# Optimization experiments

Hardware: AMD Instinct MI355X
Metric: run time of the kernel (lower is better)

The kernel has to match this reference:

```python
import jax, jax.numpy as jnp
import numpy as np

EPS = 1e-5
COORD_TAU, COORD_KAPPA = 1.0, 1.0
COT_TAU, COT_LAM = 0.8, 0.7
GATE_FLOOR = 0.05


def _gconv(x, w, b=None):
    # grouped 1x1 conv: x [B,C,H,W], w [g, co_per_g, ci_per_g]
    B, C, H, W = x.shape
    g, co, ci = w.shape
    y = jnp.einsum('goi,bgihw->bgohw', w, x.reshape(B, g, ci, H, W)).reshape(B, g * co, H, W)
    return y if b is None else y + b[None, :, None, None]


def _conv1x1(x, w):
    # dense 1x1 conv: w [Cout, Cin]
    return jnp.einsum('oi,bihw->bohw', w, x)


def _inorm(x, g, b):
    # InstanceNorm2d(affine=True): per (B,C) stats over spatial dims, biased var
    mu = x.mean(axis=(2, 3), keepdims=True)
    var = x.var(axis=(2, 3), keepdims=True)
    return (x - mu) * jax.lax.rsqrt(var + EPS) * g[None, :, None, None] + b[None, :, None, None]


def _axis_softmax(z, L, axis):
    # stabilized softmax along a spatial axis, mean-rescaled by L
    zz = z / COORD_TAU
    zz = zz - zz.max(axis=axis, keepdims=True)
    return jax.nn.softmax(zz, axis=axis) * L


def _forward(x, compress_w, inc_g, inc_b, coord_proj_w, coord_proj_g, coord_proj_b,
             coord_h_w, coord_h_b, coord_wc_w, coord_wc_b, coord_alpha, coord_beta,
             cot_key_w, cot_val_w, cot_att1_w, cot_attn_g, cot_attn_b, cot_att2_w,
             cot_fuse_w, fusion_w, fus_g, fus_b, gate_w, expand_w):
    xc = jax.nn.relu(_inorm(_conv1x1(x, compress_w), inc_g, inc_b))  # [B,m,H,W]
    B, C, H, W = xc.shape

    # ---- Coord2H branch (use_softmax=True path) ----
    def proj(t):
        return jax.nn.silu(_inorm(_gconv(t, coord_proj_w), coord_proj_g, coord_proj_b))

    zh = _gconv(proj(xc.mean(axis=3, keepdims=True)), coord_h_w, coord_h_b)   # [B,C,H,1]
    zw = _gconv(proj(xc.mean(axis=2, keepdims=True)), coord_wc_w, coord_wc_b)  # [B,C,1,W]
    ah = _axis_softmax(zh, H, 2)
    aw = _axis_softmax(zw, W, 3)
    w_lin = coord_alpha * ah + coord_beta * aw  # broadcasts to [B,C,H,W]
    coord_out = xc * (1.0 + COORD_KAPPA * (w_lin - 1.0))

    # ---- CoT branch ----
    k1 = _gconv(xc, cot_key_w)
    v = _gconv(xc, cot_val_w)
    y = jnp.concatenate([k1, xc], axis=1)  # [B,2C,H,W]
    att = jax.nn.relu(_inorm(_gconv(y, cot_att1_w), cot_attn_g, cot_attn_b))
    att_logits = _gconv(att, cot_att2_w)
    z = (att_logits / COT_TAU).reshape(B, C, H * W)
    sm = jax.nn.softmax(z - z.max(axis=-1, keepdims=True), axis=-1).reshape(B, C, H, W) * (H * W)
    att_mix = (1.0 - COT_LAM) * jax.nn.sigmoid(att_logits) + COT_LAM * sm
    cot_out = _conv1x1(k1 + att_mix * v, cot_fuse_w)

    # ---- fusion + gate + expand ----
    fused = jax.nn.relu(_inorm(_conv1x1(jnp.concatenate([coord_out, cot_out], axis=1), fusion_w), fus_g, fus_b))
    gate = jax.nn.sigmoid(jnp.einsum('oi,bi->bo', gate_w, fused.mean(axis=(2, 3))))[:, :, None, None]  # [B,1,1,1]
    return _conv1x1(fused * (gate * (1.0 - GATE_FLOOR) + GATE_FLOOR), expand_w)


def setup_inputs() -> dict:
    key = jax.random.key(0)
    B, DIM, H, W = 8, 512, 128, 128
    RED, G = 16, 4
    m = DIM // RED  # 32
    mg = m // G     # 8
    ks = jax.random.split(key, 23)

    def n(k, s, sc=0.05):
        return jax.random.normal(k, s, dtype=jnp.float32) * sc

    return {
        'x': jax.random.normal(ks[0], (B, DIM, H, W), dtype=jnp.float32),
        'compress_w': n(ks[1], (m, DIM)),
        'inc_g': 1.0 + n(ks[2], (m,)),
        'inc_b': n(ks[3], (m,)),
        'coord_proj_w': n(ks[4], (G, mg, mg), 0.2),
        'coord_proj_g': 1.0 + n(ks[5], (m,)),
        'coord_proj_b': n(ks[6], (m,)),
        'coord_h_w': n(ks[7], (G, mg, mg), 0.2),
        'coord_h_b': n(ks[8], (m,)),
        'coord_wc_w': n(ks[9], (G, mg, mg), 0.2),
        'coord_wc_b': n(ks[10], (m,)),
        'coord_alpha': jnp.asarray(0.5, dtype=jnp.float32),
        'coord_beta': jnp.asarray(0.5, dtype=jnp.float32),
        'cot_key_w': n(ks[11], (G, mg, mg), 0.2),
        'cot_val_w': n(ks[12], (G, mg, mg), 0.2),
        'cot_att1_w': n(ks[13], (G, mg, 2 * mg), 0.2),
        'cot_attn_g': 1.0 + n(ks[14], (m,)),
        'cot_attn_b': n(ks[15], (m,)),
        'cot_att2_w': n(ks[16], (G, mg, mg), 0.2),
        'cot_fuse_w': n(ks[17], (m, m), 0.1),
        'fusion_w': n(ks[18], (m, 2 * m), 0.1),
        'fus_g': 1.0 + n(ks[19], (m,)),
        'fus_b': n(ks[20], (m,)),
        'gate_w': n(ks[21], (1, m), 0.2),
        'expand_w': n(ks[22], (DIM, m), 0.1),
    }


def reference(x, compress_w, inc_g, inc_b, coord_proj_w, coord_proj_g, coord_proj_b,
              coord_h_w, coord_h_b, coord_wc_w, coord_wc_b, coord_alpha, coord_beta,
              cot_key_w, cot_val_w, cot_att1_w, cot_attn_g, cot_attn_b, cot_att2_w,
              cot_fuse_w, fusion_w, fus_g, fus_b, gate_w, expand_w):
    return _forward(x, compress_w, inc_g, inc_b, coord_proj_w, coord_proj_g, coord_proj_b,
                    coord_h_w, coord_h_b, coord_wc_w, coord_wc_b, coord_alpha, coord_beta,
                    cot_key_w, cot_val_w, cot_att1_w, cot_attn_g, cot_attn_b, cot_att2_w,
                    cot_fuse_w, fusion_w, fus_g, fus_b, gate_w, expand_w)
```

## Files before the change

kernel.cpp:

```cpp
#include <hip/hip_runtime.h>
#include <math.h>

#define NB 8
#define CIN 512
#define CM 32
#define MG 8
#define HH 128
#define WW 128
#define HWSZ (HH*WW)
#define EPSF 1e-5f
#define COT_ITAU 1.25f
#define LAM 0.7f
#define GFLOOR 0.05f

typedef float vf4 __attribute__((ext_vector_type(4)));
typedef short bf16x8 __attribute__((ext_vector_type(8)));
typedef float f32x4 __attribute__((ext_vector_type(4)));

__device__ __forceinline__ float wsum(float v){
#pragma unroll
  for (int o = 32; o; o >>= 1) v += __shfl_xor(v, o, 64);
  return v;
}

__device__ __forceinline__ unsigned short bfc(float x){
  unsigned u = __float_as_uint(x);
  return (unsigned short)((u + 0x7FFFu + ((u>>16)&1u)) >> 16);
}

__device__ __forceinline__ void gload16(const float* g, float* l){
  __builtin_amdgcn_global_load_lds(
    (const __attribute__((address_space(1))) void*)g,
    (__attribute__((address_space(3))) void*)l, 16, 0, 0);
}

__global__ void k_tw(const float* __restrict__ w, float* __restrict__ wT,
                     const float* __restrict__ ew, unsigned short* __restrict__ ewB){
  int i = blockIdx.x*256 + threadIdx.x;
  if (i < CM*CIN){
    int c = i >> 9, k = i & (CIN-1);
    wT[k*CM + c] = w[i];
    ewB[i] = bfc(ew[i]);
  }
}

__global__ __launch_bounds__(256) void k_compress(
    const float* __restrict__ x, const float* __restrict__ wT,
    float* __restrict__ y, float* __restrict__ s1, float* __restrict__ s2)
{
  __shared__ float lds[2][CM][256];
  int tid  = threadIdx.x;
  int lane = tid & 63;
  int wv   = tid >> 6;
  int b    = blockIdx.x >> 6;
  int tile0 = (blockIdx.x & 63) << 8;
  const float* xb = x + ((size_t)b*CIN)*HWSZ + tile0;

#define STAGE(t, buf)                                                        \
  {                                                                          \
    _Pragma("unroll")                                                        \
    for (int j=0;j<8;j++){                                                   \
      int ch = wv + 4*j;                                                     \
      gload16(xb + (size_t)((t)*CM + ch)*HWSZ + lane*4, &lds[buf][ch][0]);   \
    }                                                                        \
  }

  STAGE(0, 0)
  __syncthreads();

  float acc[CM];
#pragma unroll
  for (int c=0;c<CM;c++) acc[c]=0.f;

  for (int t=0; t<16; ++t){
    int cur = t & 1;
    if (t+1 < 16) STAGE(t+1, cur^1)
    const float* wr0 = wT + t*CM*CM;
#pragma unroll
    for (int i=0;i<CM;i++){
      float xv = lds[cur][i][tid];
      const float* wr = wr0 + i*CM;
#pragma unroll
      for (int c=0;c<CM;c++) acc[c] = fmaf(wr[c], xv, acc[c]);
    }
    __syncthreads();
  }
#undef STAGE

  {
    float ms=0.f, mq=0.f;
#pragma unroll
    for (int c=0;c<CM;c++){
      float s = wsum(acc[c]);
      float q = wsum(acc[c]*acc[c]);
      if ((tid&63)==c){ ms=s; mq=q; }
    }
    if (lane < CM){
      atomicAdd(&s1[b*CM+lane], ms);
      atomicAdd(&s2[b*CM+lane], mq);
    }
  }
#pragma unroll
  for (int c=0;c<CM;c++) lds[0][c][tid] = acc[c];
  __syncthreads();
  {
    vf4* yb = (vf4*)(y + ((size_t)b*CM)*HWSZ + tile0);
#pragma unroll
    for (int j=0;j<8;j++){
      int f = tid + 256*j;
      yb[(size_t)(f>>6)*(HWSZ/4) + (f&63)] = *((vf4*)&lds[0][f>>6][(f&63)*4]);
    }
  }
}

__global__ __launch_bounds__(256) void k_poolstat(
  const float* __restrict__ y,
  const float* __restrict__ s1i, const float* __restrict__ s2i,
  const float* __restrict__ incg, const float* __restrict__ incb,
  const float* __restrict__ kw, const float* __restrict__ a1w,
  float* __restrict__ s1, float* __restrict__ s2,
  float* __restrict__ hpool, float* __restrict__ wpart)
{
  __shared__ float nA[CM], nB[CM];
  __shared__ float sh[CM][128];
  int tid=threadIdx.x;
  int blk=blockIdx.x;
  int b = blk >> 6;
  int p = ((blk&63)<<8)+tid;
  if (tid<CM){
    float mu  = s1i[b*CM+tid]*(1.f/HWSZ);
    float var = fmaf(-mu,mu, s2i[b*CM+tid]*(1.f/HWSZ));
    float a   = rsqrtf(var+EPSF)*incg[tid];
    nA[tid]=a; nB[tid]=incb[tid]-mu*a;
  }
  __syncthreads();
  size_t base = ((size_t)b*CM)*HWSZ + p;
  float xc[CM], k1[CM], at[CM];
#pragma unroll
  for (int c=0;c<CM;c++)
    xc[c] = fmaxf(0.f, fmaf(y[base+(size_t)c*HWSZ], nA[c], nB[c]));
  if (tid>=128){
#pragma unroll
    for (int c=0;c<CM;c++) sh[c][tid-128]=xc[c];
  }
  __syncthreads();
  if (tid<128){
    float* wp = wpart + (size_t)blk*(CM*WW) + tid;
#pragma unroll
    for (int c=0;c<CM;c++) wp[c*WW] = xc[c] + sh[c][tid];
  }
  {
    int hrow = p >> 7;
    float ms=0.f;
#pragma unroll
    for (int c=0;c<CM;c++){
      float s=wsum(xc[c]);
      if ((tid&63)==c) ms=s;
    }
    int lane=tid&63;
    if (lane<CM) atomicAdd(&hpool[(b*CM+lane)*HH+hrow], ms*(1.f/WW));
  }
#pragma unroll
  for (int gI=0;gI<4;gI++)
#pragma unroll
    for (int o=0;o<MG;o++){
      float sk=0.f;
#pragma unroll
      for (int i=0;i<MG;i++) sk = fmaf(kw[gI*64+o*8+i], xc[gI*MG+i], sk);
      k1[gI*MG+o]=sk;
    }
#pragma unroll
  for (int gI=0;gI<4;gI++)
#pragma unroll
    for (int o=0;o<MG;o++){
      float s=0.f;
#pragma unroll
      for (int i=0;i<16;i++){
        float inp = (gI<2) ? k1[gI*16+i] : xc[(gI-2)*16+i];
        s = fmaf(a1w[gI*128+o*16+i], inp, s);
      }
      at[gI*MG+o]=s;
    }
  float ms=0.f,mq=0.f;
#pragma unroll
  for (int c=0;c<CM;c++){
    float s=wsum(at[c]); float q=wsum(at[c]*at[c]);
    if ((tid&63)==c){ms=s;mq=q;}
  }
  int lane=tid&63;
  if (lane<CM){ atomicAdd(&s1[b*CM+lane],ms); atomicAdd(&s2[b*CM+lane],mq); }
}

__global__ void k_wred(const float* __restrict__ wpart, float* __restrict__ wpool){
  int bc = blockIdx.x;
  int w  = threadIdx.x;
  int b  = bc >> 5;
  int c  = bc & 31;
  const float* src = wpart + (size_t)(b*64)*(CM*WW) + c*WW + w;
  float s=0.f;
#pragma unroll 8
  for (int k=0;k<64;k++) s += src[(size_t)k*(CM*WW)];
  wpool[bc*WW + w] = s*(1.0f/HH);
}

__global__ __launch_bounds__(256) void k_cot2(
  const float* __restrict__ y,
  const float* __restrict__ s1i, const float* __restrict__ s2i,
  const float* __restrict__ incg, const float* __restrict__ incb,
  const float* __restrict__ s1a, const float* __restrict__ s2a,
  const float* __restrict__ ag, const float* __restrict__ ab,
  const float* __restrict__ kw, const float* __restrict__ a1w, const float* __restrict__ a2w,
  const float* __restrict__ hpool, const float* __restrict__ wpool,
  const float* __restrict__ pjw, const float* __restrict__ pjg, const float* __restrict__ pjb,
  const float* __restrict__ chw, const float* __restrict__ chb,
  const float* __restrict__ cww, const float* __restrict__ cwb,
  float* __restrict__ es, float* __restrict__ ah, float* __restrict__ aw)
{
  __shared__ float T[CM][HH+1];
  __shared__ float sa[CM], sb[CM], smx[CM], ssc[CM];
  __shared__ float nA[CM], nB[CM], tA[CM], tB[CM];
  int tid=threadIdx.x;
  int blk=blockIdx.x;
  int b = blk >> 6;
  int p = ((blk&63)<<8)+tid;
  if (tid<CM){
    float mu  = s1i[b*CM+tid]*(1.f/HWSZ);
    float var = fmaf(-mu,mu, s2i[b*CM+tid]*(1.f/HWSZ));
    float a   = rsqrtf(var+EPSF)*incg[tid];
    nA[tid]=a; nB[tid]=incb[tid]-mu*a;
    float mu2  = s1a[b*CM+tid]*(1.f/HWSZ);
    float var2 = fmaf(-mu2,mu2, s2a[b*CM+tid]*(1.f/HWSZ));
    float a2   = rsqrtf(var2+EPSF)*ag[tid];
    tA[tid]=a2; tB[tid]=ab[tid]-mu2*a2;
  }
  __syncthreads();
  size_t base = ((size_t)b*CM)*HWSZ + p;
  float xc[CM], k1[CM], at[CM], l[CM];
#pragma unroll
  for (int c=0;c<CM;c++)
    xc[c] = fmaxf(0.f, fmaf(y[base+(size_t)c*HWSZ], nA[c], nB[c]));
#pragma unroll
  for (int gI=0;gI<4;gI++)
#pragma unroll
    for (int o=0;o<MG;o++){
      float sk=0.f;
#pragma unroll
      for (int i=0;i<MG;i++) sk = fmaf(kw[gI*64+o*8+i], xc[gI*MG+i], sk);
      k1[gI*MG+o]=sk;
    }
#pragma unroll
  for (int gI=0;gI<4;gI++)
#pragma unroll
    for (int o=0;o<MG;o++){
      float s=0.f;
#pragma unroll
      for (int i=0;i<16;i++){
        float inp = (gI<2) ? k1[gI*16+i] : xc[(gI-2)*16+i];
        s = fmaf(a1w[gI*128+o*16+i], inp, s);
      }
      at[gI*MG+o]=s;
    }
#pragma unroll
  for (int c=0;c<CM;c++)
    at[c] = fmaxf(0.f, fmaf(at[c], tA[c], tB[c]));
#pragma unroll
  for (int gI=0;gI<4;gI++)
#pragma unroll
    for (int o=0;o<MG;o++){
      float s=0.f;
#pragma unroll
      for (int i=0;i<MG;i++) s = fmaf(a2w[gI*64+o*8+i], at[gI*8+i], s);
      l[gI*MG+o]=s;
    }
  float ms=0.f;
#pragma unroll
  for (int c=0;c<CM;c++){
    float s = wsum(__expf(l[c]*COT_ITAU));
    if ((tid&63)==c) ms=s;
  }
  int lane=tid&63;
  if (lane<CM) atomicAdd(&es[b*CM+lane], ms);

  if (blk < 2*NB){
    int bb = blk>>1, path = blk&1;
    const float* pool = path ? wpool : hpool;
    const float* w2   = path ? cww : chw;
    const float* b2   = path ? cwb : chb;
    float* outp       = path ? aw  : ah;
    float z[CM];
    if (tid<HH){
      float in[CM];
#pragma unroll
      for (int c=0;c<CM;c++) in[c] = pool[(bb*CM+c)*HH + tid];
#pragma unroll
      for (int gI=0;gI<4;gI++)
#pragma unroll
        for (int o=0;o<MG;o++){
          float s=0.f;
#pragma unroll
          for (int i=0;i<MG;i++) s = fmaf(pjw[gI*64+o*8+i], in[gI*8+i], s);
          T[gI*8+o][tid] = s;
        }
    }
    __syncthreads();
    if (tid < CM){
      float s=0.f, q=0.f;
      for (int k=0;k<HH;k++){ float t=T[tid][k]; s+=t; q+=t*t; }
      float mu = s*(1.0f/HH);
      float var = q*(1.0f/HH) - mu*mu;
      float a = rsqrtf(var+EPSF)*pjg[tid];
      sa[tid]=a; sb[tid]=pjb[tid]-mu*a;
    }
    __syncthreads();
    if (tid<HH){
      float sil[CM];
#pragma unroll
      for (int c=0;c<CM;c++){
        float val = fmaf(T[c][tid], sa[c], sb[c]);
        sil[c] = val/(1.f+__expf(-val));
      }
#pragma unroll
      for (int gI=0;gI<4;gI++)
#pragma unroll
        for (int o=0;o<MG;o++){
          float s=b2[gI*8+o];
#pragma unroll
          for (int i=0;i<MG;i++) s = fmaf(w2[gI*64+o*8+i], sil[gI*8+i], s);
          z[gI*8+o]=s;
        }
    }
    __syncthreads();
    if (tid<HH){
#pragma unroll
      for (int c=0;c<CM;c++) T[c][tid]=z[c];
    }
    __syncthreads();
    if (tid < CM){
      float mx=-1e30f;
      for (int k=0;k<HH;k++) mx = fmaxf(mx, T[tid][k]);
      float s=0.f;
      for (int k=0;k<HH;k++) s += __expf(T[tid][k]-mx);
      smx[tid]=mx; ssc[tid]=(float)HH/s;
    }
    __syncthreads();
    if (tid<HH){
#pragma unroll
      for (int c=0;c<CM;c++)
        outp[(bb*CM+c)*HH + tid] = __expf(T[c][tid]-smx[c])*ssc[c];
    }
  }
}

__global__ __launch_bounds__(256) void k_mix_fuse(
  const float* __restrict__ y,
  const float* __restrict__ s1i, const float* __restrict__ s2i,
  const float* __restrict__ incg, const float* __restrict__ incb,
  const float* __restrict__ s1a, const float* __restrict__ s2a,
  const float* __restrict__ ag, const float* __restrict__ ab,
  const float* __restrict__ kw, const float* __restrict__ vw,
  const float* __restrict__ a1w, const float* __restrict__ a2w,
  const float* __restrict__ ah, const float* __restrict__ awp, const float* __restrict__ es,
  const float* __restrict__ alpha, const float* __restrict__ beta,
  const float* __restrict__ fw, const float* __restrict__ fuw,
  float* __restrict__ fpo, float* __restrict__ s1, float* __restrict__ s2)
{
  __shared__ float nA[CM], nB[CM], tA[CM], tB[CM];
  int tid=threadIdx.x;
  int b = blockIdx.x>>6;
  int p = ((blockIdx.x&63)<<8)+tid;
  int h = p >> 7, w = p & (WW-1);
  if (tid<CM){
    float mu  = s1i[b*CM+tid]*(1.f/HWSZ);
    float var = fmaf(-mu,mu, s2i[b*CM+tid]*(1.f/HWSZ));
    float a   = rsqrtf(var+EPSF)*incg[tid];
    nA[tid]=a; nB[tid]=incb[tid]-mu*a;
    float mu2  = s1a[b*CM+tid]*(1.f/HWSZ);
    float var2 = fmaf(-mu2,mu2, s2a[b*CM+tid]*(1.f/HWSZ));
    float a2   = rsqrtf(var2+EPSF)*ag[tid];
    tA[tid]=a2; tB[tid]=ab[tid]-mu2*a2;
  }
  __syncthreads();
  size_t base = ((size_t)b*CM)*HWSZ + p;
  float al=alpha[0], be=beta[0];
  float xc[CM], k1[CM], at[CM], l[CM], t[CM];
#pragma unroll
  for (int c=0;c<CM;c++)
    xc[c] = fmaxf(0.f, fmaf(y[base+(size_t)c*HWSZ], nA[c], nB[c]));
#pragma unroll
  for (int gI=0;gI<4;gI++)
#pragma unroll
    for (int o=0;o<MG;o++){
      float sk=0.f;
#pragma unroll
      for (int i=0;i<MG;i++) sk = fmaf(kw[gI*64+o*8+i], xc[gI*MG+i], sk);
      k1[gI*MG+o]=sk;
    }
#pragma unroll
  for (int gI=0;gI<4;gI++)
#pragma unroll
    for (int o=0;o<MG;o++){
      float s=0.f;
#pragma unroll
      for (int i=0;i<16;i++){
        float inp = (gI<2) ? k1[gI*16+i] : xc[(gI-2)*16+i];
        s = fmaf(a1w[gI*128+o*16+i], inp, s);
      }
      at[gI*MG+o]=s;
    }
#pragma unroll
  for (int c=0;c<CM;c++)
    at[c] = fmaxf(0.f, fmaf(at[c], tA[c], tB[c]));
#pragma unroll
  for (int gI=0;gI<4;gI++)
#pragma unroll
    for (int o=0;o<MG;o++){
      float s=0.f;
#pragma unroll
      for (int i=0;i<MG;i++) s = fmaf(a2w[gI*64+o*8+i], at[gI*8+i], s);
      l[gI*MG+o]=s;
    }
#pragma unroll
  for (int gI=0;gI<4;gI++)
#pragma unroll
    for (int o=0;o<MG;o++){
      float sv=0.f;
#pragma unroll
      for (int i=0;i<MG;i++) sv = fmaf(vw[gI*64+o*8+i], xc[gI*MG+i], sv);
      int c = gI*MG+o;
      float lgv = l[c];
      float sm = __expf(lgv*COT_ITAU) * (16384.f/es[b*CM+c]);
      float sg = 1.f/(1.f+__expf(-lgv));
      float mix = (1.f-LAM)*sg + LAM*sm;
      t[c] = fmaf(mix, sv, k1[c]);
    }
  float co[CM];
#pragma unroll
  for (int c=0;c<CM;c++){
    float wl = al*ah[(b*CM+c)*HH + h] + be*awp[(b*CM+c)*WW + w];
    co[c] = xc[c] * wl;
  }
  float cot[CM];
#pragma unroll
  for (int o=0;o<CM;o++){
    float s=0.f;
#pragma unroll
    for (int i=0;i<CM;i++) s = fmaf(fw[o*CM+i], t[i], s);
    cot[o]=s;
  }
  float ms=0.f, mq=0.f;
#pragma unroll
  for (int o=0;o<CM;o++){
    float s=0.f;
#pragma unroll
    for (int i=0;i<CM;i++) s = fmaf(fuw[o*64+i], co[i], s);
#pragma unroll
    for (int i=0;i<CM;i++) s = fmaf(fuw[o*64+32+i], cot[i], s);
    fpo[base+(size_t)o*HWSZ]=s;
    float ss = wsum(s); float qq = wsum(s*s);
    if ((tid&63)==o){ ms=ss; mq=qq; }
  }
  int lane=tid&63;
  if (lane<CM){ atomicAdd(&s1[b*CM+lane],ms); atomicAdd(&s2[b*CM+lane],mq); }
}

__global__ __launch_bounds__(256) void k_gstat(const float4* __restrict__ fp,
  const float* __restrict__ s1f, const float* __restrict__ s2f,
  const float* __restrict__ fg, const float* __restrict__ fb,
  float* __restrict__ gsum)
{
  int idx = blockIdx.x*256+threadIdx.x;
  int bc = idx >> 12;
  int c = bc & (CM-1);
  float mu  = s1f[bc]*(1.f/HWSZ);
  float var = fmaf(-mu,mu, s2f[bc]*(1.f/HWSZ));
  float a   = rsqrtf(var+EPSF)*fg[c];
  float bb  = fb[c]-mu*a;
  float4 tv = fp[idx];
  float s = fmaxf(0.f,fmaf(tv.x,a,bb))+fmaxf(0.f,fmaf(tv.y,a,bb))
          + fmaxf(0.f,fmaf(tv.z,a,bb))+fmaxf(0.f,fmaf(tv.w,a,bb));
  s = wsum(s);
  if ((threadIdx.x&63)==0) atomicAdd(&gsum[bc], s);
}

__global__ __launch_bounds__(256) void k_expand_mfma(
  const float* __restrict__ F,
  const float* __restrict__ s1f, const float* __restrict__ s2f,
  const float* __restrict__ fg, const float* __restrict__ fb,
  const float* __restrict__ gw, const float* __restrict__ gsum,
  const unsigned short* __restrict__ ewB, float* __restrict__ out)
{
  __shared__ float outT[128][68];
  unsigned short (*fBt)[64][8] = (unsigned short(*)[64][8])&outT[0][0];
  __shared__ float fA[CM], fB2[CM];
  int tid  = threadIdx.x;
  int lane = tid & 63;
  int wv   = tid >> 6;
  int pt   = blockIdx.x;
  int b    = blockIdx.y;
  int z    = blockIdx.z;
  int p0   = pt*64;

  if (tid<CM){
    float mu  = s1f[b*CM+tid]*(1.f/HWSZ);
    float var = fmaf(-mu,mu, s2f[b*CM+tid]*(1.f/HWSZ));
    float a   = rsqrtf(var+EPSF)*fg[tid];
    fA[tid]=a; fB2[tid]=fb[tid]-mu*a;
  }
  float gs=0.f;
#pragma unroll
  for (int c=0;c<CM;c++) gs = fmaf(gw[c], gsum[b*CM+c], gs);
  gs *= (1.0f/HWSZ);
  float sc = (1.f/(1.f+__expf(-gs)))*(1.f-GFLOOR)+GFLOOR;
  __syncthreads();

  {
    int k  = tid >> 3;
    int pb = (tid & 7) * 8;
    const float* Fb = F + ((size_t)(b*CM + k))*HWSZ + p0 + pb;
    float a = fA[k], bb = fB2[k];
    int ls_hi = (k>>3)*16;
    int j = k & 7;
#pragma unroll
    for (int u=0;u<8;u++){
      int p = pb + u;
      float v = fmaxf(0.f, fmaf(Fb[u], a, bb))*sc;
      fBt[p>>4][ls_hi + (p&15)][j] = bfc(v);
    }
  }
  __syncthreads();

  int m0 = z*128 + wv*32;
  bf16x8 a0 = *((const bf16x8*)(ewB + (size_t)(m0      + (lane&15))*CM + (lane>>4)*8));
  bf16x8 a1 = *((const bf16x8*)(ewB + (size_t)(m0 + 16 + (lane&15))*CM + (lane>>4)*8));
  f32x4 acc[2][4];
#pragma unroll
  for (int mt=0;mt<2;mt++)
#pragma unroll
    for (int t=0;t<4;t++) acc[mt][t] = (f32x4)(0.f);
#pragma unroll
  for (int t=0;t<4;t++){
    bf16x8 bb = *((const bf16x8*)&fBt[t][lane][0]);
    acc[0][t] = __builtin_amdgcn_mfma_f32_16x16x32_bf16(a0, bb, acc[0][t], 0,0,0);
    acc[1][t] = __builtin_amdgcn_mfma_f32_16x16x32_bf16(a1, bb, acc[1][t], 0,0,0);
  }
  __syncthreads();

#pragma unroll
  for (int mt=0;mt<2;mt++)
#pragma unroll
    for (int t=0;t<4;t++)
#pragma unroll
      for (int r=0;r<4;r++)
        outT[wv*32 + mt*16 + (lane>>4)*4 + r][t*16 + (lane&15)] = acc[mt][t][r];
  __syncthreads();

  {
    float* ob = out + ((size_t)(b*CIN + z*128))*HWSZ + p0;
#pragma unroll
    for (int k2=0;k2<8;k2++){
      int s = tid + 256*k2;
      int row = s >> 4, c4 = (s & 15)*4;
      vf4 v = *((vf4*)&outT[row][c4]);
      __builtin_nontemporal_store(v, (vf4*)(ob + (size_t)row*HWSZ + c4));
    }
  }
}

extern "C" void kernel_launch(void* const* d_in, const int* in_sizes, int n_in,
                              void* d_out, int out_size, void* d_ws, size_t ws_size,
                              hipStream_t stream)
{
  const float* x    = (const float*)d_in[0];
  const float* cw   = (const float*)d_in[1];
  const float* incg = (const float*)d_in[2];
  const float* incb = (const float*)d_in[3];
  const float* pjw  = (const float*)d_in[4];
  const float* pjg  = (const float*)d_in[5];
  const float* pjb  = (const float*)d_in[6];
  const float* chw  = (const float*)d_in[7];
  const float* chb  = (const float*)d_in[8];
  const float* cww  = (const float*)d_in[9];
  const float* cwb  = (const float*)d_in[10];
  const float* alpha= (const float*)d_in[11];
  const float* beta = (const float*)d_in[12];
  const float* kw   = (const float*)d_in[13];
  const float* vw   = (const float*)d_in[14];
  const float* a1w  = (const float*)d_in[15];
  const float* ag   = (const float*)d_in[16];
  const float* ab   = (const float*)d_in[17];
  const float* a2w  = (const float*)d_in[18];
  const float* fw   = (const float*)d_in[19];
  const float* fuw  = (const float*)d_in[20];
  const float* fg   = (const float*)d_in[21];
  const float* fb   = (const float*)d_in[22];
  const float* gw   = (const float*)d_in[23];
  const float* ew   = (const float*)d_in[24];
  float* out = (float*)d_out;

  float* ws = (float*)d_ws;
  const size_t BIG = (size_t)NB*CM*HWSZ;
  float* y    = ws;
  float* F    = ws +   BIG;
  float* sm   = ws + 2*BIG;
  float* acc   = sm;  sm += 2048;
  float* statS = acc,      *statQ = acc+256;
  float* attS  = acc+512,  *attQ  = acc+768;
  float* esum  = acc+1024;
  float* fusS  = acc+1280, *fusQ  = acc+1536;
  float* gsum  = acc+1792;
  float* hpool = sm;  sm += NB*CM*HH;
  float* wT    = sm;  sm += CM*CIN;
  unsigned short* ewB = (unsigned short*)sm; sm += CM*CIN/2;
  float* wpart = sm;  sm += (size_t)512*CM*WW;
  float* wpool = sm;  sm += NB*CM*WW;
  float* ahB   = sm;  sm += NB*CM*HH;
  float* awB   = sm;  sm += NB*CM*WW;

  hipMemsetAsync(acc, 0, (2048 + NB*CM*HH)*sizeof(float), stream);
  k_tw<<<64,256,0,stream>>>(cw, wT, ew, ewB);
  k_compress<<<512,256,0,stream>>>(x, wT, y, statS, statQ);
  k_poolstat<<<512,256,0,stream>>>(y,statS,statQ,incg,incb,kw,a1w,attS,attQ,hpool,wpart);
  k_wred<<<NB*CM,128,0,stream>>>(wpart, wpool);
  k_cot2<<<512,256,0,stream>>>(y,statS,statQ,incg,incb,attS,attQ,ag,ab,kw,a1w,a2w,
                               hpool,wpool,pjw,pjg,pjb,chw,chb,cww,cwb,esum,ahB,awB);
  k_mix_fuse<<<512,256,0,stream>>>(y,statS,statQ,incg,incb,attS,attQ,ag,ab,kw,vw,a1w,a2w,
                                   ahB,awB,esum,alpha,beta,fw,fuw,F,fusS,fusQ);
  k_gstat<<<4096,256,0,stream>>>((const float4*)F,fusS,fusQ,fg,fb,gsum);
  k_expand_mfma<<<dim3(256,8,4),256,0,stream>>>(F,fusS,fusQ,fg,fb,gw,gsum,ewB,out);
}
```

Measured before the change: 353.7 us.

## Use bf16 MFMA with hi/lo split for the compress 1x1 convolution

The 512->32 channel compress convolution moves from scalar FP32 FMAs to 16x16x32 bf16 MFMA instructions. Weights are pre-packed into the MFMA fragment layout as bf16. Activations are split into high and low bf16 parts so the result stays close to fp32 accuracy. The spatial tile shrinks to 128 pixels per block with twice as many blocks to raise parallelism. The cost is doubled MFMA work and per-element conversion overhead, and the weights are no longer split, so some precision is lost. The goal is to cut compute time in a kernel that reads a large input.

```diff
diff --git a/kernel.cpp b/kernel.cpp
--- a/kernel.cpp
+++ b/kernel.cpp
@@ -16,6 +16,7 @@
 typedef float vf4 __attribute__((ext_vector_type(4)));
 typedef short bf16x8 __attribute__((ext_vector_type(8)));
 typedef float f32x4 __attribute__((ext_vector_type(4)));
+typedef unsigned int u32x4 __attribute__((ext_vector_type(4)));
 
 __device__ __forceinline__ float wsum(float v){
 #pragma unroll
@@ -34,82 +35,117 @@
     (__attribute__((address_space(3))) void*)l, 16, 0, 0);
 }
 
-__global__ void k_tw(const float* __restrict__ w, float* __restrict__ wT,
+__global__ void k_tw(const float* __restrict__ cw, unsigned short* __restrict__ wF,
                      const float* __restrict__ ew, unsigned short* __restrict__ ewB){
   int i = blockIdx.x*256 + threadIdx.x;
   if (i < CM*CIN){
-    int c = i >> 9, k = i & (CIN-1);
-    wT[k*CM + c] = w[i];
+    int j = i & 7, lane = (i>>3)&63, m = (i>>9)&1, t = i>>10;
+    int c = m*16 + (lane&15);
+    int k = t*32 + ((lane>>4)<<3) + j;
+    wF[i]  = bfc(cw[c*CIN + k]);
     ewB[i] = bfc(ew[i]);
   }
 }
 
 __global__ __launch_bounds__(256) void k_compress(
-    const float* __restrict__ x, const float* __restrict__ wT,
+    const float* __restrict__ x, const unsigned short* __restrict__ wF,
     float* __restrict__ y, float* __restrict__ s1, float* __restrict__ s2)
 {
-  __shared__ float lds[2][CM][256];
+  __shared__ float xl[2][32*128];
   int tid  = threadIdx.x;
   int lane = tid & 63;
   int wv   = tid >> 6;
-  int b    = blockIdx.x >> 6;
-  int tile0 = (blockIdx.x & 63) << 8;
+  int blk  = blockIdx.x;
+  int b    = blk >> 7;
+  int tile0 = (blk & 127) << 7;
   const float* xb = x + ((size_t)b*CIN)*HWSZ + tile0;
 
-#define STAGE(t, buf)                                                        \
-  {                                                                          \
-    _Pragma("unroll")                                                        \
-    for (int j=0;j<8;j++){                                                   \
-      int ch = wv + 4*j;                                                     \
-      gload16(xb + (size_t)((t)*CM + ch)*HWSZ + lane*4, &lds[buf][ch][0]);   \
-    }                                                                        \
+#define STAGE(t, buf)                                                           \
+  {                                                                             \
+    _Pragma("unroll")                                                           \
+    for (int j=0;j<4;j++){                                                      \
+      int ch2 = j*8 + wv*2;                                                     \
+      gload16(xb + (size_t)((t)*CM + ch2 + (lane>>5))*HWSZ + (lane&31)*4,       \
+              &xl[buf][ch2*128]);                                               \
+    }                                                                           \
   }
 
   STAGE(0, 0)
   __syncthreads();
 
-  float acc[CM];
-#pragma unroll
-  for (int c=0;c<CM;c++) acc[c]=0.f;
+  f32x4 acc[2][2];
+#pragma unroll
+  for (int m=0;m<2;m++)
+#pragma unroll
+    for (int nt=0;nt<2;nt++) acc[m][nt] = (f32x4)(0.f);
 
   for (int t=0; t<16; ++t){
     int cur = t & 1;
     if (t+1 < 16) STAGE(t+1, cur^1)
-    const float* wr0 = wT + t*CM*CM;
-#pragma unroll
-    for (int i=0;i<CM;i++){
-      float xv = lds[cur][i][tid];
-      const float* wr = wr0 + i*CM;
-#pragma unroll
-      for (int c=0;c<CM;c++) acc[c] = fmaf(wr[c], xv, acc[c]);
+    bf16x8 a0 = *((const bf16x8*)(wF + ((size_t)(t*2+0)*64 + lane)*8));
+    bf16x8 a1 = *((const bf16x8*)(wF + ((size_t)(t*2+1)*64 + lane)*8));
+#pragma unroll
+    for (int nt=0;nt<2;nt++){
+      int col = wv*32 + nt*16 + (lane&15);
+      int r0  = (lane>>4)*8;
+      u32x4 hw, lw;
+#pragma unroll
+      for (int wd=0; wd<4; wd++){
+        float f0 = xl[cur][(r0+2*wd  )*128 + col];
+        float f1 = xl[cur][(r0+2*wd+1)*128 + col];
+        unsigned short h0=bfc(f0), h1=bfc(f1);
+        float e0 = f0 - __uint_as_float(((unsigned)h0)<<16);
+        float e1 = f1 - __uint_as_float(((unsigned)h1)<<16);
+        hw[wd] = (unsigned)h0 | (((unsigned)h1)<<16);
+        lw[wd] = (unsigned)bfc(e0) | (((unsigned)bfc(e1))<<16);
+      }
+      bf16x8 bh = __builtin_bit_cast(bf16x8, hw);
+      bf16x8 bl = __builtin_bit_cast(bf16x8, lw);
+      if (nt==0){
+        acc[0][0] = __builtin_amdgcn_mfma_f32_16x16x32_bf16(a0, bh, acc[0][0], 0,0,0);
+        acc[0][0] = __builtin_amdgcn_mfma_f32_16x16x32_bf16(a0, bl, acc[0][0], 0,0,0);
+        acc[1][0] = __builtin_amdgcn_mfma_f32_16x16x32_bf16(a1, bh, acc[1][0], 0,0,0);
+        acc[1][0] = __builtin_amdgcn_mfma_f32_16x16x32_bf16(a1, bl, acc[1][0], 0,0,0);
+      } else {
+        acc[0][1] = __builtin_amdgcn_mfma_f32_16x16x32_bf16(a0, bh, acc[0][1], 0,0,0);
+        acc[0][1] = __builtin_amdgcn_mfma_f32_16x16x32_bf16(a0, bl, acc[0][1], 0,0,0);
+        acc[1][1] = __builtin_amdgcn_mfma_f32_16x16x32_bf16(a1, bh, acc[1][1], 0,0,0);
+        acc[1][1] = __builtin_amdgcn_mfma_f32_16x16x32_bf16(a1, bl, acc[1][1], 0,0,0);
+      }
     }
     __syncthreads();
   }
 #undef STAGE
 
-  {
-    float ms=0.f, mq=0.f;
-#pragma unroll
-    for (int c=0;c<CM;c++){
-      float s = wsum(acc[c]);
-      float q = wsum(acc[c]*acc[c]);
-      if ((tid&63)==c){ ms=s; mq=q; }
-    }
-    if (lane < CM){
-      atomicAdd(&s1[b*CM+lane], ms);
-      atomicAdd(&s2[b*CM+lane], mq);
-    }
-  }
-#pragma unroll
-  for (int c=0;c<CM;c++) lds[0][c][tid] = acc[c];
-  __syncthreads();
-  {
-    vf4* yb = (vf4*)(y + ((size_t)b*CM)*HWSZ + tile0);
-#pragma unroll
-    for (int j=0;j<8;j++){
-      int f = tid + 256*j;
-      yb[(size_t)(f>>6)*(HWSZ/4) + (f&63)] = *((vf4*)&lds[0][f>>6][(f&63)*4]);
-    }
+#pragma unroll
+  for (int m=0;m<2;m++)
+#pragma unroll
+    for (int r=0;r<4;r++){
+      float s = acc[m][0][r] + acc[m][1][r];
+      float q = acc[m][0][r]*acc[m][0][r] + acc[m][1][r]*acc[m][1][r];
+#pragma unroll
+      for (int o=1;o<16;o<<=1){ s += __shfl_xor(s,o,64); q += __shfl_xor(q,o,64); }
+      if ((lane&15)==0){
+        int c = m*16 + (lane>>4)*4 + r;
+        atomicAdd(&s1[b*CM+c], s);
+        atomicAdd(&s2[b*CM+c], q);
+      }
+    }
+
+  float* yl = &xl[0][0];
+#pragma unroll
+  for (int m=0;m<2;m++)
+#pragma unroll
+    for (int nt=0;nt<2;nt++)
+#pragma unroll
+      for (int r=0;r<4;r++)
+        yl[(m*16 + (lane>>4)*4 + r)*128 + wv*32 + nt*16 + (lane&15)] = acc[m][nt][r];
+  __syncthreads();
+#pragma unroll
+  for (int k2=0;k2<4;k2++){
+    int s = tid + 256*k2;
+    int row = s >> 5, c4s = s & 31;
+    ((vf4*)(y + ((size_t)(b*CM+row))*HWSZ + tile0))[c4s] = *((vf4*)&yl[row*128 + c4s*4]);
   }
 }
 
@@ -609,7 +645,7 @@
   float* fusS  = acc+1280, *fusQ  = acc+1536;
   float* gsum  = acc+1792;
   float* hpool = sm;  sm += NB*CM*HH;
-  float* wT    = sm;  sm += CM*CIN;
+  unsigned short* wF  = (unsigned short*)sm; sm += CM*CIN/2;
   unsigned short* ewB = (unsigned short*)sm; sm += CM*CIN/2;
   float* wpart = sm;  sm += (size_t)512*CM*WW;
   float* wpool = sm;  sm += NB*CM*WW;
@@ -617,8 +653,8 @@
   float* awB   = sm;  sm += NB*CM*WW;
 
   hipMemsetAsync(acc, 0, (2048 + NB*CM*HH)*sizeof(float), stream);
-  k_tw<<<64,256,0,stream>>>(cw, wT, ew, ewB);
-  k_compress<<<512,256,0,stream>>>(x, wT, y, statS, statQ);
+  k_tw<<<64,256,0,stream>>>(cw, wF, ew, ewB);
+  k_compress<<<1024,256,0,stream>>>(x, wF, y, statS, statQ);
   k_poolstat<<<512,256,0,stream>>>(y,statS,statQ,incg,incb,kw,a1w,attS,attQ,hpool,wpart);
   k_wred<<<NB*CM,128,0,stream>>>(wpart, wpool);
   k_cot2<<<512,256,0,stream>>>(y,statS,statQ,incg,incb,attS,attQ,ag,ab,kw,a1w,a2w,
```

Measured after the change: 348.6 us (median of 2 runs). No clear change (-1.4%).

## Store compressed and fused intermediates channel-last (NHWC) for vectorized per-pixel access

Applied to the files above, without the earlier changes.

Switches the intermediate tensors y and F from channel-planar [B,C,HW] to pixel-major [B,HW,C]. Each thread can then write and read its 32 channels with eight 16-byte vector accesses instead of 32 strided scalar accesses, and k_compress drops its LDS transpose and barrier. k_gstat now folds the gate weights into a single per-batch sum and runs with fewer blocks, which moves the gate dot product out of k_expand. The risk is that the 128-byte per-thread stride makes each wave's access uncoalesced within a single instruction, and the gsum layout changes to one value per batch.

```diff
diff --git a/kernel.cpp b/kernel.cpp
--- a/kernel.cpp
+++ b/kernel.cpp
@@ -46,7 +46,7 @@
 
 __global__ __launch_bounds__(256) void k_compress(
     const float* __restrict__ x, const float* __restrict__ wT,
-    float* __restrict__ y, float* __restrict__ s1, float* __restrict__ s2)
+    float* __restrict__ y2, float* __restrict__ s1, float* __restrict__ s2)
 {
   __shared__ float lds[2][CM][256];
   int tid  = threadIdx.x;
@@ -100,21 +100,18 @@
       atomicAdd(&s2[b*CM+lane], mq);
     }
   }
-#pragma unroll
-  for (int c=0;c<CM;c++) lds[0][c][tid] = acc[c];
-  __syncthreads();
-  {
-    vf4* yb = (vf4*)(y + ((size_t)b*CM)*HWSZ + tile0);
-#pragma unroll
-    for (int j=0;j<8;j++){
-      int f = tid + 256*j;
-      yb[(size_t)(f>>6)*(HWSZ/4) + (f&63)] = *((vf4*)&lds[0][f>>6][(f&63)*4]);
+  {
+    vf4* yp = (vf4*)(y2 + ((size_t)b*HWSZ + tile0 + tid)*CM);
+#pragma unroll
+    for (int k=0;k<8;k++){
+      vf4 v; v.x=acc[4*k]; v.y=acc[4*k+1]; v.z=acc[4*k+2]; v.w=acc[4*k+3];
+      yp[k] = v;
     }
   }
 }
 
 __global__ __launch_bounds__(256) void k_poolstat(
-  const float* __restrict__ y,
+  const float* __restrict__ y2,
   const float* __restrict__ s1i, const float* __restrict__ s2i,
   const float* __restrict__ incg, const float* __restrict__ incb,
   const float* __restrict__ kw, const float* __restrict__ a1w,
@@ -134,11 +131,18 @@
     nA[tid]=a; nB[tid]=incb[tid]-mu*a;
   }
   __syncthreads();
-  size_t base = ((size_t)b*CM)*HWSZ + p;
   float xc[CM], k1[CM], at[CM];
-#pragma unroll
-  for (int c=0;c<CM;c++)
-    xc[c] = fmaxf(0.f, fmaf(y[base+(size_t)c*HWSZ], nA[c], nB[c]));
+  {
+    const vf4* yp = (const vf4*)(y2 + ((size_t)b*HWSZ + p)*CM);
+#pragma unroll
+    for (int k=0;k<8;k++){
+      vf4 v = yp[k];
+      xc[4*k]   = fmaxf(0.f, fmaf(v.x, nA[4*k],   nB[4*k]));
+      xc[4*k+1] = fmaxf(0.f, fmaf(v.y, nA[4*k+1], nB[4*k+1]));
+      xc[4*k+2] = fmaxf(0.f, fmaf(v.z, nA[4*k+2], nB[4*k+2]));
+      xc[4*k+3] = fmaxf(0.f, fmaf(v.w, nA[4*k+3], nB[4*k+3]));
+    }
+  }
   if (tid>=128){
 #pragma unroll
     for (int c=0;c<CM;c++) sh[c][tid-128]=xc[c];
@@ -204,7 +208,7 @@
 }
 
 __global__ __launch_bounds__(256) void k_cot2(
-  const float* __restrict__ y,
+  const float* __restrict__ y2,
   const float* __restrict__ s1i, const float* __restrict__ s2i,
   const float* __restrict__ incg, const float* __restrict__ incb,
   const float* __restrict__ s1a, const float* __restrict__ s2a,
@@ -234,11 +238,18 @@
     tA[tid]=a2; tB[tid]=ab[tid]-mu2*a2;
   }
   __syncthreads();
-  size_t base = ((size_t)b*CM)*HWSZ + p;
   float xc[CM], k1[CM], at[CM], l[CM];
-#pragma unroll
-  for (int c=0;c<CM;c++)
-    xc[c] = fmaxf(0.f, fmaf(y[base+(size_t)c*HWSZ], nA[c], nB[c]));
+  {
+    const vf4* yp = (const vf4*)(y2 + ((size_t)b*HWSZ + p)*CM);
+#pragma unroll
+    for (int k=0;k<8;k++){
+      vf4 v = yp[k];
+      xc[4*k]   = fmaxf(0.f, fmaf(v.x, nA[4*k],   nB[4*k]));
+      xc[4*k+1] = fmaxf(0.f, fmaf(v.y, nA[4*k+1], nB[4*k+1]));
+      xc[4*k+2] = fmaxf(0.f, fmaf(v.z, nA[4*k+2], nB[4*k+2]));
+      xc[4*k+3] = fmaxf(0.f, fmaf(v.w, nA[4*k+3], nB[4*k+3]));
+    }
+  }
 #pragma unroll
   for (int gI=0;gI<4;gI++)
 #pragma unroll
@@ -352,7 +363,7 @@
 }
 
 __global__ __launch_bounds__(256) void k_mix_fuse(
-  const float* __restrict__ y,
+  const float* __restrict__ y2,
   const float* __restrict__ s1i, const float* __restrict__ s2i,
   const float* __restrict__ incg, const float* __restrict__ incb,
   const float* __restrict__ s1a, const float* __restrict__ s2a,
@@ -362,7 +373,7 @@
   const float* __restrict__ ah, const float* __restrict__ awp, const float* __restrict__ es,
   const float* __restrict__ alpha, const float* __restrict__ beta,
   const float* __restrict__ fw, const float* __restrict__ fuw,
-  float* __restrict__ fpo, float* __restrict__ s1, float* __restrict__ s2)
+  float* __restrict__ F2, float* __restrict__ s1, float* __restrict__ s2)
 {
   __shared__ float nA[CM], nB[CM], tA[CM], tB[CM];
   int tid=threadIdx.x;
@@ -380,12 +391,19 @@
     tA[tid]=a2; tB[tid]=ab[tid]-mu2*a2;
   }
   __syncthreads();
-  size_t base = ((size_t)b*CM)*HWSZ + p;
   float al=alpha[0], be=beta[0];
   float xc[CM], k1[CM], at[CM], l[CM], t[CM];
-#pragma unroll
-  for (int c=0;c<CM;c++)
-    xc[c] = fmaxf(0.f, fmaf(y[base+(size_t)c*HWSZ], nA[c], nB[c]));
+  {
+    const vf4* yp = (const vf4*)(y2 + ((size_t)b*HWSZ + p)*CM);
+#pragma unroll
+    for (int k=0;k<8;k++){
+      vf4 v = yp[k];
+      xc[4*k]   = fmaxf(0.f, fmaf(v.x, nA[4*k],   nB[4*k]));
+      xc[4*k+1] = fmaxf(0.f, fmaf(v.y, nA[4*k+1], nB[4*k+1]));
+      xc[4*k+2] = fmaxf(0.f, fmaf(v.z, nA[4*k+2], nB[4*k+2]));
+      xc[4*k+3] = fmaxf(0.f, fmaf(v.w, nA[4*k+3], nB[4*k+3]));
+    }
+  }
 #pragma unroll
   for (int gI=0;gI<4;gI++)
 #pragma unroll
@@ -447,6 +465,7 @@
     for (int i=0;i<CM;i++) s = fmaf(fw[o*CM+i], t[i], s);
     cot[o]=s;
   }
+  float fus[CM];
   float ms=0.f, mq=0.f;
 #pragma unroll
   for (int o=0;o<CM;o++){
@@ -455,38 +474,59 @@
     for (int i=0;i<CM;i++) s = fmaf(fuw[o*64+i], co[i], s);
 #pragma unroll
     for (int i=0;i<CM;i++) s = fmaf(fuw[o*64+32+i], cot[i], s);
-    fpo[base+(size_t)o*HWSZ]=s;
+    fus[o]=s;
     float ss = wsum(s); float qq = wsum(s*s);
     if ((tid&63)==o){ ms=ss; mq=qq; }
   }
   int lane=tid&63;
   if (lane<CM){ atomicAdd(&s1[b*CM+lane],ms); atomicAdd(&s2[b*CM+lane],mq); }
-}
-
-__global__ __launch_bounds__(256) void k_gstat(const float4* __restrict__ fp,
+  {
+    vf4* fp = (vf4*)(F2 + ((size_t)b*HWSZ + p)*CM);
+#pragma unroll
+    for (int k=0;k<8;k++){
+      vf4 v; v.x=fus[4*k]; v.y=fus[4*k+1]; v.z=fus[4*k+2]; v.w=fus[4*k+3];
+      fp[k] = v;
+    }
+  }
+}
+
+__global__ __launch_bounds__(256) void k_gstat(const float* __restrict__ F2,
   const float* __restrict__ s1f, const float* __restrict__ s2f,
   const float* __restrict__ fg, const float* __restrict__ fb,
-  float* __restrict__ gsum)
+  const float* __restrict__ gw, float* __restrict__ gsum)
 {
-  int idx = blockIdx.x*256+threadIdx.x;
-  int bc = idx >> 12;
-  int c = bc & (CM-1);
-  float mu  = s1f[bc]*(1.f/HWSZ);
-  float var = fmaf(-mu,mu, s2f[bc]*(1.f/HWSZ));
-  float a   = rsqrtf(var+EPSF)*fg[c];
-  float bb  = fb[c]-mu*a;
-  float4 tv = fp[idx];
-  float s = fmaxf(0.f,fmaf(tv.x,a,bb))+fmaxf(0.f,fmaf(tv.y,a,bb))
-          + fmaxf(0.f,fmaf(tv.z,a,bb))+fmaxf(0.f,fmaf(tv.w,a,bb));
+  __shared__ float fA[CM], fB2[CM], gwl[CM];
+  int tid=threadIdx.x;
+  int blk=blockIdx.x;
+  int b = blk >> 6;
+  int p = ((blk&63)<<8)+tid;
+  if (tid<CM){
+    float mu  = s1f[b*CM+tid]*(1.f/HWSZ);
+    float var = fmaf(-mu,mu, s2f[b*CM+tid]*(1.f/HWSZ));
+    float a   = rsqrtf(var+EPSF)*fg[tid];
+    fA[tid]=a; fB2[tid]=fb[tid]-mu*a;
+    gwl[tid]=gw[tid];
+  }
+  __syncthreads();
+  const vf4* fp = (const vf4*)(F2 + ((size_t)b*HWSZ + p)*CM);
+  float s=0.f;
+#pragma unroll
+  for (int k=0;k<8;k++){
+    vf4 v = fp[k];
+    s = fmaf(gwl[4*k],   fmaxf(0.f, fmaf(v.x, fA[4*k],   fB2[4*k])),   s);
+    s = fmaf(gwl[4*k+1], fmaxf(0.f, fmaf(v.y, fA[4*k+1], fB2[4*k+1])), s);
+    s = fmaf(gwl[4*k+2], fmaxf(0.f, fmaf(v.z, fA[4*k+2], fB2[4*k+2])), s);
+    s = fmaf(gwl[4*k+3], fmaxf(0.f, fmaf(v.w, fA[4*k+3], fB2[4*k+3])), s);
+  }
   s = wsum(s);
-  if ((threadIdx.x&63)==0) atomicAdd(&gsum[bc], s);
+  if ((tid&63)==0) atomicAdd(&gsum[b], s);
 }
 
 __global__ __launch_bounds__(256) void k_expand_mfma(
-  const float* __restrict__ F,
+  const float* __restrict__ F2,
   const float* __restrict__ s1f, const float* __restrict__ s2f,
   const float* __restrict__ fg, const float* __restrict__ fb,
-  const float* __restrict__ gw, const float* __restrict__ gsum,
+  const float* __restrict__ gsum,
   const unsigned short* __restrict__ ewB, float* __restrict__ out)
 {
   __shared__ float outT[128][68];
@@ -506,25 +546,21 @@
     float a   = rsqrtf(var+EPSF)*fg[tid];
     fA[tid]=a; fB2[tid]=fb[tid]-mu*a;
   }
-  float gs=0.f;
-#pragma unroll
-  for (int c=0;c<CM;c++) gs = fmaf(gw[c], gsum[b*CM+c], gs);
-  gs *= (1.0f/HWSZ);
+  float gs = gsum[b]*(1.0f/HWSZ);
   float sc = (1.f/(1.f+__expf(-gs)))*(1.f-GFLOOR)+GFLOOR;
   __syncthreads();
 
   {
-    int k  = tid >> 3;
-    int pb = (tid & 7) * 8;
-    const float* Fb = F + ((size_t)(b*CM + k))*HWSZ + p0 + pb;
-    float a = fA[k], bb = fB2[k];
-    int ls_hi = (k>>3)*16;
-    int j = k & 7;
-#pragma unroll
-    for (int u=0;u<8;u++){
-      int p = pb + u;
-      float v = fmaxf(0.f, fmaf(Fb[u], a, bb))*sc;
-      fBt[p>>4][ls_hi + (p&15)][j] = bfc(v);
+    int pl = tid & 63;
+    int g  = tid >> 6;
+    const vf4* Fp = (const vf4*)(F2 + ((size_t)b*HWSZ + p0 + pl)*CM + g*8);
+    vf4 v0 = Fp[0], v1 = Fp[1];
+    float vv[8] = {v0.x,v0.y,v0.z,v0.w,v1.x,v1.y,v1.z,v1.w};
+#pragma unroll
+    for (int j=0;j<8;j++){
+      int k = g*8+j;
+      float val = fmaxf(0.f, fmaf(vv[j], fA[k], fB2[k]))*sc;
+      fBt[pl>>4][g*16 + (pl&15)][j] = bfc(val);
     }
   }
   __syncthreads();
@@ -625,6 +661,6 @@
                                hpool,wpool,pjw,pjg,pjb,chw,chb,cww,cwb,esum,ahB,awB);
   k_mix_fuse<<<512,256,0,stream>>>(y,statS,statQ,incg,incb,attS,attQ,ag,ab,kw,vw,a1w,a2w,
                                    ahB,awB,esum,alpha,beta,fw,fuw,F,fusS,fusQ);
-  k_gstat<<<4096,256,0,stream>>>((const float4*)F,fusS,fusQ,fg,fb,gsum);
-  k_expand_mfma<<<dim3(256,8,4),256,0,stream>>>(F,fusS,fusQ,fg,fb,gw,gsum,ewB,out);
-}
+  k_gstat<<<512,256,0,stream>>>(F,fusS,fusQ,fg,fb,gw,gsum);
+  k_expand_mfma<<<dim3(256,8,4),256,0,stream>>>(F,fusS,fusQ,fg,fb,gsum,ewB,out);
+}
```

Result: no change. 360.0 us (+1.8%).
